# Kernel tuning notes

Hardware: AMD Instinct MI355X
Metric: run time of the kernel (lower is better)

## Reference

```python
import jax, jax.numpy as jnp
import numpy as np

D_E = 128
D_R = 128  # must equal D_E for the original torch code to typecheck
BN_EPS = 1e-5


def setup_inputs() -> dict:
    key = jax.random.key(0)
    ks = jax.random.split(key, 8)
    B, S = 16, 2048
    h = jax.random.normal(ks[0], (B, S, D_E), dtype=jnp.float32)
    r = jax.random.normal(ks[1], (B, S, D_R), dtype=jnp.float32)
    t = jax.random.normal(ks[2], (B, S, D_E), dtype=jnp.float32)
    # Xavier-uniform core tensor W: (d_r, d_e, d_e)
    limit = float(np.sqrt(6.0 / (D_R + D_E * D_E)))
    W = jax.random.uniform(ks[3], (D_R, D_E, D_E), minval=-limit, maxval=limit, dtype=jnp.float32)
    # BatchNorm1d params/buffers (inference mode)
    gamma0 = jnp.ones((D_E,), jnp.float32)
    beta0 = jnp.zeros((D_E,), jnp.float32)
    mean0 = 0.1 * jax.random.normal(ks[4], (D_E,), dtype=jnp.float32)
    var0 = jnp.abs(1.0 + 0.1 * jax.random.normal(ks[5], (D_E,), dtype=jnp.float32))
    gamma1 = jnp.ones((D_E,), jnp.float32)
    beta1 = jnp.zeros((D_E,), jnp.float32)
    mean1 = 0.1 * jax.random.normal(ks[6], (D_E,), dtype=jnp.float32)
    var1 = jnp.abs(1.0 + 0.1 * jax.random.normal(ks[7], (D_E,), dtype=jnp.float32))
    return {"h": h, "r": r, "t": t, "W": W,
            "gamma0": gamma0, "beta0": beta0, "mean0": mean0, "var0": var0,
            "gamma1": gamma1, "beta1": beta1, "mean1": mean1, "var1": var1}


def reference(h, r, t, W, gamma0, beta0, mean0, var0, gamma1, beta1, mean1, var1):
    B, S, D = h.shape  # D == d_e == d_r
    N = B * S
    # BatchNorm1d in eval mode over last dim; dropout is identity in eval.
    h_bn = (h - mean0) * jax.lax.rsqrt(var0 + BN_EPS) * gamma0 + beta0
    t_bn = (t - mean1) * jax.lax.rsqrt(var1 + BN_EPS) * gamma1 + beta1
    r2 = r.reshape(N, D)
    # torch.matmul((N,d_r), (d_r,d_e,d_e)) broadcasts -> shape (d_r, N, d_e):
    #   out[k, n, j] = sum_i r2[n, i] * W[k, i, j]
    # followed by .view(N, d_e, d_e) which reinterprets the flat buffer.
    W_mat = jnp.einsum('ni,kij->knj', r2, W).reshape(N, D, D)  # (N, d_e, d_e) after scrambled view
    # hr[n, j] = sum_d h_bn[n, d] * W_mat[n, d, j]
    hr = jnp.einsum('nd,ndj->nj', h_bn.reshape(N, D), W_mat)
    scores = jnp.sum(hr * t_bn.reshape(N, D), axis=-1)  # (N,)
    return scores.reshape(B, S)
```

## Files before the change

### kernel.cpp

```cpp
#include <hip/hip_runtime.h>


typedef __attribute__((ext_vector_type(8))) short bf16x8;
typedef __attribute__((ext_vector_type(4))) short s16x4;
typedef __attribute__((ext_vector_type(4))) float f32x4;

#define DPAD 136
#define BN_EPS 1e-5f

__device__ inline unsigned short f2bf(float f) {
  unsigned u = __builtin_bit_cast(unsigned, f);
  u += 0x7FFFu + ((u >> 16) & 1u);
  return (unsigned short)(u >> 16);
}
__device__ inline float bf2f(unsigned short h) {
  unsigned u = ((unsigned)h) << 16;
  return __builtin_bit_cast(float, u);
}
__device__ inline unsigned pack2bf(float lo, float hi) {
  return (unsigned)f2bf(lo) | ((unsigned)f2bf(hi) << 16);
}

__global__ __launch_bounds__(256) void k_uv(
    const float* __restrict__ h, const float* __restrict__ r,
    const float* __restrict__ t, const float* __restrict__ W,
    const float* __restrict__ gamma0, const float* __restrict__ beta0,
    const float* __restrict__ mean0, const float* __restrict__ var0,
    const float* __restrict__ gamma1, const float* __restrict__ beta1,
    const float* __restrict__ mean1, const float* __restrict__ var1,
    unsigned short* __restrict__ V, unsigned short* __restrict__ U) {
  __shared__ short LA[128 * DPAD];
  __shared__ short LB[128 * DPAD];
  const int tid = threadIdx.x;
  const int c = tid & 31;
  const int rr = tid >> 5;
  const int wv_ = tid >> 6;
  const int lane = tid & 63;
  const int l16 = lane & 15;
  const int quad = lane >> 4;

  f32x4 acc[2][8];
  for (int mt = 0; mt < 2; ++mt)
    for (int nt = 0; nt < 8; ++nt) acc[mt][nt] = (f32x4){0.f, 0.f, 0.f, 0.f};

  if (blockIdx.x < 256) {
    const int k = blockIdx.x >> 1;
    const int half = blockIdx.x & 1;
    const int rowbase = k * 256 + half * 128;

    f32x4 g  = *(const f32x4*)(gamma1 + c * 4);
    f32x4 be = *(const f32x4*)(beta1  + c * 4);
    f32x4 mu = *(const f32x4*)(mean1  + c * 4);
    f32x4 va = *(const f32x4*)(var1   + c * 4);
    f32x4 sc, bi;
    for (int q = 0; q < 4; ++q) {
      sc[q] = g[q] * rsqrtf(va[q] + BN_EPS);
      bi[q] = be[q] - mu[q] * sc[q];
    }
    const float* tbase = t + (size_t)rowbase * 128;
    const float* wbase = W + (size_t)k * 16384;
    for (int it = 0; it < 16; ++it) {
      const int m = it * 8 + rr;
      f32x4 tv = *(const f32x4*)(tbase + m * 128 + c * 4);
      s16x4 tb;
      for (int q = 0; q < 4; ++q) tb[q] = (short)f2bf(tv[q] * sc[q] + bi[q]);
      *(s16x4*)(&LA[m * DPAD + c * 4]) = tb;
      f32x4 wvv = *(const f32x4*)(wbase + m * 128 + c * 4);
      s16x4 wb;
      for (int q = 0; q < 4; ++q) wb[q] = (short)f2bf(wvv[q]);
      *(s16x4*)(&LB[m * DPAD + c * 4]) = wb;
    }
    __syncthreads();

    for (int ks = 0; ks < 4; ++ks) {
      const int K0 = ks * 32 + quad * 8;
      bf16x8 a[2], b[8];
      for (int mt = 0; mt < 2; ++mt)
        a[mt] = *(const bf16x8*)(&LA[(wv_ * 32 + mt * 16 + l16) * DPAD + K0]);
      for (int nt = 0; nt < 8; ++nt)
        b[nt] = *(const bf16x8*)(&LB[(nt * 16 + l16) * DPAD + K0]);
      for (int mt = 0; mt < 2; ++mt)
        for (int nt = 0; nt < 8; ++nt)
          acc[mt][nt] = __builtin_amdgcn_mfma_f32_16x16x32_bf16(b[nt], a[mt], acc[mt][nt], 0, 0, 0);
    }

    for (int mt = 0; mt < 2; ++mt) {
      const size_t np = (size_t)(rowbase + wv_ * 32 + mt * 16 + l16) * 128;
      for (int nt = 0; nt < 8; ++nt) {
        unsigned two[2];
        two[0] = pack2bf(acc[mt][nt][0], acc[mt][nt][1]);
        two[1] = pack2bf(acc[mt][nt][2], acc[mt][nt][3]);
        *(uint2*)(V + np + nt * 16 + quad * 4) = *(uint2*)two;
      }
    }
  } else {
    const int low = blockIdx.x - 256;

    f32x4 g  = *(const f32x4*)(gamma0 + c * 4);
    f32x4 be = *(const f32x4*)(beta0  + c * 4);
    f32x4 mu = *(const f32x4*)(mean0  + c * 4);
    f32x4 va = *(const f32x4*)(var0   + c * 4);
    f32x4 sc, bi;
    for (int q = 0; q < 4; ++q) {
      sc[q] = g[q] * rsqrtf(va[q] + BN_EPS);
      bi[q] = be[q] - mu[q] * sc[q];
    }
    for (int it = 0; it < 16; ++it) {
      const int kk = it * 8 + rr;
      f32x4 hv = *(const f32x4*)(h + ((size_t)(kk * 256 + low)) * 128 + c * 4);
      s16x4 hb;
      for (int q = 0; q < 4; ++q) hb[q] = (short)f2bf(hv[q] * sc[q] + bi[q]);
      *(s16x4*)(&LA[kk * DPAD + c * 4]) = hb;
    }
    for (int it = 0; it < 4; ++it) {
      const int a0 = it * 32 + rr * 4;
      f32x4 rv[4];
      for (int v = 0; v < 4; ++v)
        rv[v] = *(const f32x4*)(r + ((size_t)(low * 128 + a0 + v)) * 128 + c * 4);
      for (int u = 0; u < 4; ++u) {
        s16x4 w;
        for (int v = 0; v < 4; ++v) w[v] = (short)f2bf(rv[v][u]);
        *(s16x4*)(&LB[(c * 4 + u) * DPAD + a0]) = w;
      }
    }
    __syncthreads();

    for (int ks = 0; ks < 4; ++ks) {
      const int K0 = ks * 32 + quad * 8;
      bf16x8 a[2], b[8];
      for (int mt = 0; mt < 2; ++mt)
        a[mt] = *(const bf16x8*)(&LA[(wv_ * 32 + mt * 16 + l16) * DPAD + K0]);
      for (int nt = 0; nt < 8; ++nt)
        b[nt] = *(const bf16x8*)(&LB[(nt * 16 + l16) * DPAD + K0]);
      for (int mt = 0; mt < 2; ++mt)
        for (int nt = 0; nt < 8; ++nt)
          acc[mt][nt] = __builtin_amdgcn_mfma_f32_16x16x32_bf16(b[nt], a[mt], acc[mt][nt], 0, 0, 0);
    }

    for (int mt = 0; mt < 2; ++mt) {
      const size_t np = ((size_t)(wv_ * 32 + mt * 16 + l16) * 256 + low) * 128;
      for (int nt = 0; nt < 8; ++nt) {
        unsigned two[2];
        two[0] = pack2bf(acc[mt][nt][0], acc[mt][nt][1]);
        two[1] = pack2bf(acc[mt][nt][2], acc[mt][nt][3]);
        *(uint2*)(U + np + nt * 16 + quad * 4) = *(uint2*)two;
      }
    }
  }
}

__global__ __launch_bounds__(256) void k_dot(
    const unsigned short* __restrict__ U, const unsigned short* __restrict__ V,
    float* __restrict__ out) {
  const int tid = threadIdx.x;
  const int row = blockIdx.x * 16 + (tid >> 4);
  const int l = tid & 15;
  const uint4 uv = *(const uint4*)(U + (size_t)row * 128 + l * 8);
  const uint4 vv = *(const uint4*)(V + (size_t)row * 128 + l * 8);
  const unsigned* up = (const unsigned*)&uv;
  const unsigned* vp = (const unsigned*)&vv;
  float s = 0.f;
  for (int q = 0; q < 4; ++q) {
    unsigned a = up[q], b = vp[q];
    s += bf2f((unsigned short)(a & 0xFFFFu)) * bf2f((unsigned short)(b & 0xFFFFu));
    s += bf2f((unsigned short)(a >> 16)) * bf2f((unsigned short)(b >> 16));
  }
  for (int m = 1; m < 16; m <<= 1) s += __shfl_xor(s, m, 16);
  if (l == 0) out[row] = s;
}

extern "C" void kernel_launch(void* const* d_in, const int* in_sizes, int n_in,
                              void* d_out, int out_size, void* d_ws, size_t ws_size,
                              hipStream_t stream) {
  const float* h      = (const float*)d_in[0];
  const float* r      = (const float*)d_in[1];
  const float* t      = (const float*)d_in[2];
  const float* W      = (const float*)d_in[3];
  const float* gamma0 = (const float*)d_in[4];
  const float* beta0  = (const float*)d_in[5];
  const float* mean0  = (const float*)d_in[6];
  const float* var0   = (const float*)d_in[7];
  const float* gamma1 = (const float*)d_in[8];
  const float* beta1  = (const float*)d_in[9];
  const float* mean1  = (const float*)d_in[10];
  const float* var1   = (const float*)d_in[11];
  float* out = (float*)d_out;

  unsigned short* V = (unsigned short*)d_ws;
  unsigned short* U = V + (size_t)32768 * 128;

  k_uv<<<512, 256, 0, stream>>>(h, r, t, W,
                                gamma0, beta0, mean0, var0,
                                gamma1, beta1, mean1, var1, V, U);
  k_dot<<<2048, 256, 0, stream>>>(U, V, out);
}
```

Before: 116.8 us.

## Fuse U-side GEMM with final dot product to drop U buffer

Splits the combined kernel into a V-producing stage and a second kernel that computes the U tile and immediately dots it with V in registers, writing scores directly. This removes the U bf16 round trip through global memory and the separate dot-product kernel. The cost is serialising the U computation after V (256 blocks each instead of 512 concurrent), which may reduce parallelism.

```diff
diff --git a/kernel.cpp b/kernel.cpp
--- a/kernel.cpp
+++ b/kernel.cpp
@@ -21,14 +21,11 @@
   return (unsigned)f2bf(lo) | ((unsigned)f2bf(hi) << 16);
 }
 
-__global__ __launch_bounds__(256) void k_uv(
-    const float* __restrict__ h, const float* __restrict__ r,
+__global__ __launch_bounds__(256) void k_stageA(
     const float* __restrict__ t, const float* __restrict__ W,
-    const float* __restrict__ gamma0, const float* __restrict__ beta0,
-    const float* __restrict__ mean0, const float* __restrict__ var0,
     const float* __restrict__ gamma1, const float* __restrict__ beta1,
     const float* __restrict__ mean1, const float* __restrict__ var1,
-    unsigned short* __restrict__ V, unsigned short* __restrict__ U) {
+    unsigned short* __restrict__ V) {
   __shared__ short LA[128 * DPAD];
   __shared__ short LB[128 * DPAD];
   const int tid = threadIdx.x;
@@ -39,134 +36,138 @@
   const int l16 = lane & 15;
   const int quad = lane >> 4;
 
+  const int k = blockIdx.x >> 1;
+  const int half = blockIdx.x & 1;
+  const int rowbase = k * 256 + half * 128;
+
+  f32x4 g  = *(const f32x4*)(gamma1 + c * 4);
+  f32x4 be = *(const f32x4*)(beta1  + c * 4);
+  f32x4 mu = *(const f32x4*)(mean1  + c * 4);
+  f32x4 va = *(const f32x4*)(var1   + c * 4);
+  f32x4 sc, bi;
+  for (int q = 0; q < 4; ++q) {
+    sc[q] = g[q] * rsqrtf(va[q] + BN_EPS);
+    bi[q] = be[q] - mu[q] * sc[q];
+  }
+  const float* tbase = t + (size_t)rowbase * 128;
+  const float* wbase = W + (size_t)k * 16384;
+  for (int it = 0; it < 16; ++it) {
+    const int m = it * 8 + rr;
+    f32x4 tv = *(const f32x4*)(tbase + m * 128 + c * 4);
+    s16x4 tb;
+    for (int q = 0; q < 4; ++q) tb[q] = (short)f2bf(tv[q] * sc[q] + bi[q]);
+    *(s16x4*)(&LA[m * DPAD + c * 4]) = tb;
+    f32x4 wvv = *(const f32x4*)(wbase + m * 128 + c * 4);
+    s16x4 wb;
+    for (int q = 0; q < 4; ++q) wb[q] = (short)f2bf(wvv[q]);
+    *(s16x4*)(&LB[m * DPAD + c * 4]) = wb;
+  }
+  __syncthreads();
+
   f32x4 acc[2][8];
   for (int mt = 0; mt < 2; ++mt)
     for (int nt = 0; nt < 8; ++nt) acc[mt][nt] = (f32x4){0.f, 0.f, 0.f, 0.f};
 
-  if (blockIdx.x < 256) {
-    const int k = blockIdx.x >> 1;
-    const int half = blockIdx.x & 1;
-    const int rowbase = k * 256 + half * 128;
+  for (int ks = 0; ks < 4; ++ks) {
+    const int K0 = ks * 32 + quad * 8;
+    bf16x8 a[2], b[8];
+    for (int mt = 0; mt < 2; ++mt)
+      a[mt] = *(const bf16x8*)(&LA[(wv_ * 32 + mt * 16 + l16) * DPAD + K0]);
+    for (int nt = 0; nt < 8; ++nt)
+      b[nt] = *(const bf16x8*)(&LB[(nt * 16 + l16) * DPAD + K0]);
+    for (int mt = 0; mt < 2; ++mt)
+      for (int nt = 0; nt < 8; ++nt)
+        acc[mt][nt] = __builtin_amdgcn_mfma_f32_16x16x32_bf16(b[nt], a[mt], acc[mt][nt], 0, 0, 0);
+  }
 
-    f32x4 g  = *(const f32x4*)(gamma1 + c * 4);
-    f32x4 be = *(const f32x4*)(beta1  + c * 4);
-    f32x4 mu = *(const f32x4*)(mean1  + c * 4);
-    f32x4 va = *(const f32x4*)(var1   + c * 4);
-    f32x4 sc, bi;
-    for (int q = 0; q < 4; ++q) {
-      sc[q] = g[q] * rsqrtf(va[q] + BN_EPS);
-      bi[q] = be[q] - mu[q] * sc[q];
-    }
-    const float* tbase = t + (size_t)rowbase * 128;
-    const float* wbase = W + (size_t)k * 16384;
-    for (int it = 0; it < 16; ++it) {
-      const int m = it * 8 + rr;
-      f32x4 tv = *(const f32x4*)(tbase + m * 128 + c * 4);
-      s16x4 tb;
-      for (int q = 0; q < 4; ++q) tb[q] = (short)f2bf(tv[q] * sc[q] + bi[q]);
-      *(s16x4*)(&LA[m * DPAD + c * 4]) = tb;
-      f32x4 wvv = *(const f32x4*)(wbase + m * 128 + c * 4);
-      s16x4 wb;
-      for (int q = 0; q < 4; ++q) wb[q] = (short)f2bf(wvv[q]);
-      *(s16x4*)(&LB[m * DPAD + c * 4]) = wb;
-    }
-    __syncthreads();
-
-    for (int ks = 0; ks < 4; ++ks) {
-      const int K0 = ks * 32 + quad * 8;
-      bf16x8 a[2], b[8];
-      for (int mt = 0; mt < 2; ++mt)
-        a[mt] = *(const bf16x8*)(&LA[(wv_ * 32 + mt * 16 + l16) * DPAD + K0]);
-      for (int nt = 0; nt < 8; ++nt)
-        b[nt] = *(const bf16x8*)(&LB[(nt * 16 + l16) * DPAD + K0]);
-      for (int mt = 0; mt < 2; ++mt)
-        for (int nt = 0; nt < 8; ++nt)
-          acc[mt][nt] = __builtin_amdgcn_mfma_f32_16x16x32_bf16(b[nt], a[mt], acc[mt][nt], 0, 0, 0);
-    }
-
-    for (int mt = 0; mt < 2; ++mt) {
-      const size_t np = (size_t)(rowbase + wv_ * 32 + mt * 16 + l16) * 128;
-      for (int nt = 0; nt < 8; ++nt) {
-        unsigned two[2];
-        two[0] = pack2bf(acc[mt][nt][0], acc[mt][nt][1]);
-        two[1] = pack2bf(acc[mt][nt][2], acc[mt][nt][3]);
-        *(uint2*)(V + np + nt * 16 + quad * 4) = *(uint2*)two;
-      }
-    }
-  } else {
-    const int low = blockIdx.x - 256;
-
-    f32x4 g  = *(const f32x4*)(gamma0 + c * 4);
-    f32x4 be = *(const f32x4*)(beta0  + c * 4);
-    f32x4 mu = *(const f32x4*)(mean0  + c * 4);
-    f32x4 va = *(const f32x4*)(var0   + c * 4);
-    f32x4 sc, bi;
-    for (int q = 0; q < 4; ++q) {
-      sc[q] = g[q] * rsqrtf(va[q] + BN_EPS);
-      bi[q] = be[q] - mu[q] * sc[q];
-    }
-    for (int it = 0; it < 16; ++it) {
-      const int kk = it * 8 + rr;
-      f32x4 hv = *(const f32x4*)(h + ((size_t)(kk * 256 + low)) * 128 + c * 4);
-      s16x4 hb;
-      for (int q = 0; q < 4; ++q) hb[q] = (short)f2bf(hv[q] * sc[q] + bi[q]);
-      *(s16x4*)(&LA[kk * DPAD + c * 4]) = hb;
-    }
-    for (int it = 0; it < 4; ++it) {
-      const int a0 = it * 32 + rr * 4;
-      f32x4 rv[4];
-      for (int v = 0; v < 4; ++v)
-        rv[v] = *(const f32x4*)(r + ((size_t)(low * 128 + a0 + v)) * 128 + c * 4);
-      for (int u = 0; u < 4; ++u) {
-        s16x4 w;
-        for (int v = 0; v < 4; ++v) w[v] = (short)f2bf(rv[v][u]);
-        *(s16x4*)(&LB[(c * 4 + u) * DPAD + a0]) = w;
-      }
-    }
-    __syncthreads();
-
-    for (int ks = 0; ks < 4; ++ks) {
-      const int K0 = ks * 32 + quad * 8;
-      bf16x8 a[2], b[8];
-      for (int mt = 0; mt < 2; ++mt)
-        a[mt] = *(const bf16x8*)(&LA[(wv_ * 32 + mt * 16 + l16) * DPAD + K0]);
-      for (int nt = 0; nt < 8; ++nt)
-        b[nt] = *(const bf16x8*)(&LB[(nt * 16 + l16) * DPAD + K0]);
-      for (int mt = 0; mt < 2; ++mt)
-        for (int nt = 0; nt < 8; ++nt)
-          acc[mt][nt] = __builtin_amdgcn_mfma_f32_16x16x32_bf16(b[nt], a[mt], acc[mt][nt], 0, 0, 0);
-    }
-
-    for (int mt = 0; mt < 2; ++mt) {
-      const size_t np = ((size_t)(wv_ * 32 + mt * 16 + l16) * 256 + low) * 128;
-      for (int nt = 0; nt < 8; ++nt) {
-        unsigned two[2];
-        two[0] = pack2bf(acc[mt][nt][0], acc[mt][nt][1]);
-        two[1] = pack2bf(acc[mt][nt][2], acc[mt][nt][3]);
-        *(uint2*)(U + np + nt * 16 + quad * 4) = *(uint2*)two;
-      }
+  for (int mt = 0; mt < 2; ++mt) {
+    const size_t np = (size_t)(rowbase + wv_ * 32 + mt * 16 + l16) * 128;
+    for (int nt = 0; nt < 8; ++nt) {
+      unsigned two[2];
+      two[0] = pack2bf(acc[mt][nt][0], acc[mt][nt][1]);
+      two[1] = pack2bf(acc[mt][nt][2], acc[mt][nt][3]);
+      *(uint2*)(V + np + nt * 16 + quad * 4) = *(uint2*)two;
     }
   }
 }
 
-__global__ __launch_bounds__(256) void k_dot(
-    const unsigned short* __restrict__ U, const unsigned short* __restrict__ V,
-    float* __restrict__ out) {
+__global__ __launch_bounds__(256) void k_bdot(
+    const float* __restrict__ h, const float* __restrict__ r,
+    const float* __restrict__ gamma0, const float* __restrict__ beta0,
+    const float* __restrict__ mean0, const float* __restrict__ var0,
+    const unsigned short* __restrict__ V, float* __restrict__ out) {
+  __shared__ short LA[128 * DPAD];
+  __shared__ short LB[128 * DPAD];
   const int tid = threadIdx.x;
-  const int row = blockIdx.x * 16 + (tid >> 4);
-  const int l = tid & 15;
-  const uint4 uv = *(const uint4*)(U + (size_t)row * 128 + l * 8);
-  const uint4 vv = *(const uint4*)(V + (size_t)row * 128 + l * 8);
-  const unsigned* up = (const unsigned*)&uv;
-  const unsigned* vp = (const unsigned*)&vv;
-  float s = 0.f;
+  const int c = tid & 31;
+  const int rr = tid >> 5;
+  const int wv_ = tid >> 6;
+  const int lane = tid & 63;
+  const int l16 = lane & 15;
+  const int quad = lane >> 4;
+
+  const int low = blockIdx.x;
+
+  f32x4 g  = *(const f32x4*)(gamma0 + c * 4);
+  f32x4 be = *(const f32x4*)(beta0  + c * 4);
+  f32x4 mu = *(const f32x4*)(mean0  + c * 4);
+  f32x4 va = *(const f32x4*)(var0   + c * 4);
+  f32x4 sc, bi;
   for (int q = 0; q < 4; ++q) {
-    unsigned a = up[q], b = vp[q];
-    s += bf2f((unsigned short)(a & 0xFFFFu)) * bf2f((unsigned short)(b & 0xFFFFu));
-    s += bf2f((unsigned short)(a >> 16)) * bf2f((unsigned short)(b >> 16));
+    sc[q] = g[q] * rsqrtf(va[q] + BN_EPS);
+    bi[q] = be[q] - mu[q] * sc[q];
   }
-  for (int m = 1; m < 16; m <<= 1) s += __shfl_xor(s, m, 16);
-  if (l == 0) out[row] = s;
+  for (int it = 0; it < 16; ++it) {
+    const int kk = it * 8 + rr;
+    f32x4 hv = *(const f32x4*)(h + ((size_t)(kk * 256 + low)) * 128 + c * 4);
+    s16x4 hb;
+    for (int q = 0; q < 4; ++q) hb[q] = (short)f2bf(hv[q] * sc[q] + bi[q]);
+    *(s16x4*)(&LA[kk * DPAD + c * 4]) = hb;
+  }
+  for (int it = 0; it < 4; ++it) {
+    const int a0 = it * 32 + rr * 4;
+    f32x4 rv[4];
+    for (int v = 0; v < 4; ++v)
+      rv[v] = *(const f32x4*)(r + ((size_t)(low * 128 + a0 + v)) * 128 + c * 4);
+    for (int u = 0; u < 4; ++u) {
+      s16x4 w;
+      for (int v = 0; v < 4; ++v) w[v] = (short)f2bf(rv[v][u]);
+      *(s16x4*)(&LB[(c * 4 + u) * DPAD + a0]) = w;
+    }
+  }
+  __syncthreads();
+
+  f32x4 acc[2][8];
+  for (int mt = 0; mt < 2; ++mt)
+    for (int nt = 0; nt < 8; ++nt) acc[mt][nt] = (f32x4){0.f, 0.f, 0.f, 0.f};
+
+  for (int ks = 0; ks < 4; ++ks) {
+    const int K0 = ks * 32 + quad * 8;
+    bf16x8 a[2], b[8];
+    for (int mt = 0; mt < 2; ++mt)
+      a[mt] = *(const bf16x8*)(&LA[(wv_ * 32 + mt * 16 + l16) * DPAD + K0]);
+    for (int nt = 0; nt < 8; ++nt)
+      b[nt] = *(const bf16x8*)(&LB[(nt * 16 + l16) * DPAD + K0]);
+    for (int mt = 0; mt < 2; ++mt)
+      for (int nt = 0; nt < 8; ++nt)
+        acc[mt][nt] = __builtin_amdgcn_mfma_f32_16x16x32_bf16(b[nt], a[mt], acc[mt][nt], 0, 0, 0);
+  }
+
+  for (int mt = 0; mt < 2; ++mt) {
+    const int kk = wv_ * 32 + mt * 16 + l16;
+    const size_t np = ((size_t)kk * 256 + low) * 128;
+    float s = 0.f;
+    for (int nt = 0; nt < 8; ++nt) {
+      const uint2 vv = *(const uint2*)(V + np + nt * 16 + quad * 4);
+      s += acc[mt][nt][0] * bf2f((unsigned short)(vv.x & 0xFFFFu));
+      s += acc[mt][nt][1] * bf2f((unsigned short)(vv.x >> 16));
+      s += acc[mt][nt][2] * bf2f((unsigned short)(vv.y & 0xFFFFu));
+      s += acc[mt][nt][3] * bf2f((unsigned short)(vv.y >> 16));
+    }
+    s += __shfl_xor(s, 16, 64);
+    s += __shfl_xor(s, 32, 64);
+    if (quad == 0) out[(size_t)kk * 256 + low] = s;
+  }
 }
 
 extern "C" void kernel_launch(void* const* d_in, const int* in_sizes, int n_in,
@@ -187,10 +188,7 @@
   float* out = (float*)d_out;
 
   unsigned short* V = (unsigned short*)d_ws;
-  unsigned short* U = V + (size_t)32768 * 128;
 
-  k_uv<<<512, 256, 0, stream>>>(h, r, t, W,
-                                gamma0, beta0, mean0, var0,
-                                gamma1, beta1, mean1, var1, V, U);
-  k_dot<<<2048, 256, 0, stream>>>(U, V, out);
+  k_stageA<<<256, 256, 0, stream>>>(t, W, gamma1, beta1, mean1, var1, V);
+  k_bdot<<<256, 256, 0, stream>>>(h, r, gamma0, beta0, mean0, var0, V, out);
 }
```

Result: no change. 115.1 us (-1.5%).
